# Performance work log

Measured on AMD Instinct MI355X. Metric: run time of the kernel, lower is better.

Reference implementation:

```python
import jax, jax.numpy as jnp
import numpy as np
import math

HIDDEN = 2048
NUM_HEADS = 32
NUM_KV_HEADS = 8
HEAD_DIM = HIDDEN // NUM_HEADS
GROUPS = NUM_HEADS // NUM_KV_HEADS
B, S = 2, 2048


def setup_inputs() -> dict:
    key = jax.random.key(0)
    ks = jax.random.split(key, 9)
    sc = 1.0 / math.sqrt(HIDDEN)
    x = jax.random.normal(ks[0], (B, S, HIDDEN), dtype=jnp.float32)
    # causal mask: 1 where attention allowed, 0 where masked
    mask = jnp.tril(jnp.ones((S, S), dtype=jnp.int32))[None, None, :, :]
    Wq = jax.random.normal(ks[1], (HIDDEN, HIDDEN), dtype=jnp.float32) * sc
    bq = jnp.zeros((HIDDEN,), dtype=jnp.float32)
    Wk = jax.random.normal(ks[2], (NUM_KV_HEADS * HEAD_DIM, HIDDEN), dtype=jnp.float32) * sc
    bk = jnp.zeros((NUM_KV_HEADS * HEAD_DIM,), dtype=jnp.float32)
    Wv = jax.random.normal(ks[3], (NUM_KV_HEADS * HEAD_DIM, HIDDEN), dtype=jnp.float32) * sc
    bv = jnp.zeros((NUM_KV_HEADS * HEAD_DIM,), dtype=jnp.float32)
    Wo = jax.random.normal(ks[4], (HIDDEN, HIDDEN), dtype=jnp.float32) * sc
    bo = jnp.zeros((HIDDEN,), dtype=jnp.float32)
    return {"x": x, "mask": mask, "Wq": Wq, "bq": bq, "Wk": Wk, "bk": bk,
            "Wv": Wv, "bv": bv, "Wo": Wo, "bo": bo}


def reference(x, mask, Wq, bq, Wk, bk, Wv, bv, Wo, bo):
    b, s, _ = x.shape
    # projections (torch Linear: y = x @ W.T + b)
    Q = (x @ Wq.T + bq).reshape(b, s, NUM_HEADS, HEAD_DIM).transpose(0, 2, 1, 3)  # b h s d
    K = (x @ Wk.T + bk).reshape(b, s, NUM_KV_HEADS, HEAD_DIM).transpose(0, 2, 1, 3)
    V = (x @ Wv.T + bv).reshape(b, s, NUM_KV_HEADS, HEAD_DIM).transpose(0, 2, 1, 3)
    # repeat_kv expansion
    K = jnp.repeat(K, GROUPS, axis=1)  # b h s d
    V = jnp.repeat(V, GROUPS, axis=1)
    scores = jnp.einsum('bhqd,bhkd->bhqk', Q, K) / math.sqrt(HEAD_DIM)
    scores = jnp.where(mask == 0, jnp.float32(-jnp.inf), scores)
    w = jax.nn.softmax(scores, axis=-1)
    # dropout is identity in eval mode
    out = jnp.einsum('bhqk,bhkd->bhqd', w, V)
    out = out.transpose(0, 2, 1, 3).reshape(b, s, HIDDEN)
    return out @ Wo.T + bo
```

## Files before the change

### kernel.cpp

```cpp
#include <hip/hip_runtime.h>
#include <hip/hip_bf16.h>
#include <stdint.h>

#define HID   2048
#define SLEN  2048
#define NB    2
#define NHEADS 32
#define NKVH   8
#define HDIM   64
#define KVW    512

typedef __bf16 bf16_t;
typedef __bf16 bf16x4 __attribute__((ext_vector_type(4)));
typedef __bf16 bf16x8 __attribute__((ext_vector_type(8)));
typedef float  f32x4  __attribute__((ext_vector_type(4)));

__device__ __forceinline__ f32x4 mfma16(bf16x8 a, bf16x8 b, f32x4 c) {
  return __builtin_amdgcn_mfma_f32_16x16x32_bf16(a, b, c, 0, 0, 0);
}

__device__ __forceinline__ void gl2lds16(const bf16_t* g, bf16_t* l) {
  __builtin_amdgcn_global_load_lds(
      (const __attribute__((address_space(1))) void*)g,
      (__attribute__((address_space(3))) void*)l,
      16, 0, 0);
}

__device__ __forceinline__ float fast_exp2(float x) {
#if __has_builtin(__builtin_amdgcn_exp2f)
  return __builtin_amdgcn_exp2f(x);
#else
  return __expf(x * 0.69314718f);
#endif
}

__device__ __forceinline__ bf16x8 ld8(const bf16_t* p) {
  return *(const bf16x8*)p;
}
__device__ __forceinline__ bf16x8 ld8(const float* p) {
  f32x4 a = *(const f32x4*)p;
  f32x4 b = *(const f32x4*)(p + 4);
  bf16x8 r;
  r[0] = (bf16_t)a[0]; r[1] = (bf16_t)a[1]; r[2] = (bf16_t)a[2]; r[3] = (bf16_t)a[3];
  r[4] = (bf16_t)b[0]; r[5] = (bf16_t)b[1]; r[6] = (bf16_t)b[2]; r[7] = (bf16_t)b[3];
  return r;
}

__device__ __forceinline__ void st_c(bf16_t* p, float v) { *p = (bf16_t)v; }
__device__ __forceinline__ void st_c(float*  p, float v) { *p = v; }

__global__ __launch_bounds__(256) void cvt_kernel(
    const float* __restrict__ x,  const float* __restrict__ wq,
    const float* __restrict__ wk, const float* __restrict__ wv,
    const float* __restrict__ wo,
    bf16_t* xb, bf16_t* wqb, bf16_t* wkb, bf16_t* wvb, bf16_t* wob)
{
  const float* s; bf16_t* d; size_t n;
  switch (blockIdx.y) {
    case 0:  s = x;  d = xb;  n = (size_t)NB * SLEN * HID; break;
    case 1:  s = wq; d = wqb; n = (size_t)HID * HID; break;
    case 2:  s = wk; d = wkb; n = (size_t)KVW * HID; break;
    case 3:  s = wv; d = wvb; n = (size_t)KVW * HID; break;
    default: s = wo; d = wob; n = (size_t)HID * HID; break;
  }
  const size_t stride = (size_t)gridDim.x * 256 * 8;
  for (size_t i = ((size_t)blockIdx.x * 256 + threadIdx.x) * 8; i < n; i += stride)
    *(bf16x8*)(d + i) = ld8(s + i);
}


__device__ __forceinline__ bf16x8 ldfrag(const bf16_t* __restrict__ Lh, int r, int g) {
  return *(const bf16x8*)(Lh + r * 64 + ((g ^ (r & 7)) << 3));
}

template <int Q>
__device__ __forceinline__ void mfma_quad(const bf16x8 (&af)[2][2],
                                          const bf16x8 (&bfr)[4][2],
                                          f32x4 (&acc)[8][4]) {
#pragma unroll
  for (int ks = 0; ks < 2; ++ks)
#pragma unroll
    for (int i = 0; i < 2; ++i)
#pragma unroll
      for (int ni = 0; ni < 4; ++ni)
        acc[2 * Q + i][ni] = mfma16(af[i][ks], bfr[ni][ks], acc[2 * Q + i][ni]);
}

__device__ __forceinline__ void phase_barrier() {
  __builtin_amdgcn_s_barrier();
  asm volatile("" ::: "memory");
}

__device__ __forceinline__ void gemm256_core(
    const bf16_t* __restrict__ Ag,
    const bf16_t* __restrict__ Bg,
    bf16_t* __restrict__ lds, f32x4 (&acc)[8][4])
{
  const int tid  = threadIdx.x;
  const int lane = tid & 63;
  const int w    = tid >> 6;
  const int fr   = lane & 15;
  const int quad = lane >> 4;
  const int wr   = w >> 2;
  const int wc   = w & 3;
  const int rbB  = (wc & 1) * 64;

  bf16_t* A0 = lds;
  bf16_t* B0 = lds + 16384;
  bf16_t* A1 = lds + 32768;
  bf16_t* B1 = lds + 49152;
  const bf16_t* Ar0 = A0 + wr * 8192;
  const bf16_t* Br0 = B0 + (wc >> 1) * 8192;
  const bf16_t* Ar1 = A1 + wr * 8192;
  const bf16_t* Br1 = B1 + (wc >> 1) * 8192;

  const f32x4 z4 = {0.f, 0.f, 0.f, 0.f};
#pragma unroll
  for (int i = 0; i < 8; ++i)
#pragma unroll
    for (int j = 0; j < 4; ++j) acc[i][j] = z4;

  auto STAGE = [&](const bf16_t* __restrict__ Gp, bf16_t* __restrict__ Lh) {
#pragma unroll
    for (int j = 0; j < 2; ++j) {
      const int s = j * 512 + tid;
      const int r = s >> 3;
      const int g = (s & 7) ^ (r & 7);
      gl2lds16(Gp + (size_t)r * HID + g * 8, Lh + s * 8);
    }
  };

  STAGE(Bg,                  B0);
  STAGE(Bg + 128 * HID,      B0 + 8192);
  STAGE(Ag,                  A0);
  STAGE(Ag + 128 * HID,      A0 + 8192);
  STAGE(Bg + 64,             B1);
  STAGE(Bg + 128 * HID + 64, B1 + 8192);
  asm volatile("s_waitcnt vmcnt(4)" ::: "memory");
  phase_barrier();

  bf16x8 bfr[4][2], af[2][2];

#pragma unroll 1
  for (int it = 0; it < 16; ++it) {
    const bool more = (it < 15);
    const size_t k1 = (size_t)(2 * it + 1) * 64;
    const size_t k2 = (size_t)(2 * it + 2) * 64;
    const size_t k3 = (size_t)(2 * it + 3) * 64;

#pragma unroll
    for (int ni = 0; ni < 4; ++ni)
#pragma unroll
      for (int ks = 0; ks < 2; ++ks)
        bfr[ni][ks] = ldfrag(Br0, rbB + ni * 16 + fr, ks * 4 + quad);
#pragma unroll
    for (int i = 0; i < 2; ++i)
#pragma unroll
      for (int ks = 0; ks < 2; ++ks)
        af[i][ks] = ldfrag(Ar0, i * 16 + fr, ks * 4 + quad);
    STAGE(Ag + k1, A1);
    phase_barrier();
    asm volatile("s_waitcnt lgkmcnt(0)" ::: "memory");
    __builtin_amdgcn_s_setprio(1);
    mfma_quad<0>(af, bfr, acc);
    __builtin_amdgcn_s_setprio(0);
    phase_barrier();

#pragma unroll
    for (int i = 0; i < 2; ++i)
#pragma unroll
      for (int ks = 0; ks < 2; ++ks)
        af[i][ks] = ldfrag(Ar0, 32 + i * 16 + fr, ks * 4 + quad);
    STAGE(Ag + 128 * HID + k1, A1 + 8192);
    phase_barrier();
    asm volatile("s_waitcnt lgkmcnt(0)" ::: "memory");
    __builtin_amdgcn_s_setprio(1);
    mfma_quad<1>(af, bfr, acc);
    __builtin_amdgcn_s_setprio(0);
    phase_barrier();

#pragma unroll
    for (int i = 0; i < 2; ++i)
#pragma unroll
      for (int ks = 0; ks < 2; ++ks)
        af[i][ks] = ldfrag(Ar0, 64 + i * 16 + fr, ks * 4 + quad);
    if (more) STAGE(Bg + k2, B0);
    phase_barrier();
    asm volatile("s_waitcnt lgkmcnt(0)" ::: "memory");
    __builtin_amdgcn_s_setprio(1);
    mfma_quad<2>(af, bfr, acc);
    __builtin_amdgcn_s_setprio(0);
    phase_barrier();

#pragma unroll
    for (int i = 0; i < 2; ++i)
#pragma unroll
      for (int ks = 0; ks < 2; ++ks)
        af[i][ks] = ldfrag(Ar0, 96 + i * 16 + fr, ks * 4 + quad);
    if (more) STAGE(Bg + 128 * HID + k2, B0 + 8192);
    phase_barrier();
    asm volatile("s_waitcnt lgkmcnt(0)" ::: "memory");
    __builtin_amdgcn_s_setprio(1);
    mfma_quad<3>(af, bfr, acc);
    __builtin_amdgcn_s_setprio(0);
    if (more) { asm volatile("s_waitcnt vmcnt(4)" ::: "memory"); }
    else      { asm volatile("s_waitcnt vmcnt(0)" ::: "memory"); }
    phase_barrier();

#pragma unroll
    for (int ni = 0; ni < 4; ++ni)
#pragma unroll
      for (int ks = 0; ks < 2; ++ks)
        bfr[ni][ks] = ldfrag(Br1, rbB + ni * 16 + fr, ks * 4 + quad);
#pragma unroll
    for (int i = 0; i < 2; ++i)
#pragma unroll
      for (int ks = 0; ks < 2; ++ks)
        af[i][ks] = ldfrag(Ar1, i * 16 + fr, ks * 4 + quad);
    if (more) STAGE(Ag + k2, A0);
    phase_barrier();
    asm volatile("s_waitcnt lgkmcnt(0)" ::: "memory");
    __builtin_amdgcn_s_setprio(1);
    mfma_quad<0>(af, bfr, acc);
    __builtin_amdgcn_s_setprio(0);
    phase_barrier();

#pragma unroll
    for (int i = 0; i < 2; ++i)
#pragma unroll
      for (int ks = 0; ks < 2; ++ks)
        af[i][ks] = ldfrag(Ar1, 32 + i * 16 + fr, ks * 4 + quad);
    if (more) STAGE(Ag + 128 * HID + k2, A0 + 8192);
    phase_barrier();
    asm volatile("s_waitcnt lgkmcnt(0)" ::: "memory");
    __builtin_amdgcn_s_setprio(1);
    mfma_quad<1>(af, bfr, acc);
    __builtin_amdgcn_s_setprio(0);
    phase_barrier();

#pragma unroll
    for (int i = 0; i < 2; ++i)
#pragma unroll
      for (int ks = 0; ks < 2; ++ks)
        af[i][ks] = ldfrag(Ar1, 64 + i * 16 + fr, ks * 4 + quad);
    if (more) STAGE(Bg + k3, B1);
    phase_barrier();
    asm volatile("s_waitcnt lgkmcnt(0)" ::: "memory");
    __builtin_amdgcn_s_setprio(1);
    mfma_quad<2>(af, bfr, acc);
    __builtin_amdgcn_s_setprio(0);
    phase_barrier();

#pragma unroll
    for (int i = 0; i < 2; ++i)
#pragma unroll
      for (int ks = 0; ks < 2; ++ks)
        af[i][ks] = ldfrag(Ar1, 96 + i * 16 + fr, ks * 4 + quad);
    if (more) STAGE(Bg + 128 * HID + k3, B1 + 8192);
    phase_barrier();
    asm volatile("s_waitcnt lgkmcnt(0)" ::: "memory");
    __builtin_amdgcn_s_setprio(1);
    mfma_quad<3>(af, bfr, acc);
    __builtin_amdgcn_s_setprio(0);
    if (more) { asm volatile("s_waitcnt vmcnt(4)" ::: "memory"); }
    phase_barrier();
  }
}

__global__ __launch_bounds__(512, 2) void qkv8_kernel(
    const bf16_t* __restrict__ xb, const bf16_t* __restrict__ Wcat,
    const float* __restrict__ bcat,
    bf16_t* __restrict__ Qb, bf16_t* __restrict__ Kb, bf16_t* __restrict__ VbT)
{
  __shared__ __align__(16) bf16_t lds[65536];
  const int cb = blockIdx.x;
  const int mb = blockIdx.y;
  f32x4 acc[8][4];
  gemm256_core(xb + (size_t)mb * 256 * HID, Wcat + (size_t)cb * 256 * HID, lds, acc);

  const int tid = threadIdx.x, lane = tid & 63, w = tid >> 6;
  const int fr = lane & 15, quad = lane >> 4, wr = w >> 2, wc = w & 3;
#pragma unroll
  for (int ni = 0; ni < 4; ++ni) {
    const int gcol = cb * 256 + wc * 64 + ni * 16 + fr;
    const float bz = bcat[gcol];
#pragma unroll
    for (int mi = 0; mi < 8; ++mi) {
      const int grow = mb * 256 + wr * 128 + mi * 16 + quad * 4;
      if (cb < 8) {
#pragma unroll
        for (int r = 0; r < 4; ++r)
          Qb[(size_t)(grow + r) * HID + gcol] = (bf16_t)(acc[mi][ni][r] + bz);
      } else if (cb < 10) {
        const int kc = gcol - 2048;
#pragma unroll
        for (int r = 0; r < 4; ++r)
          Kb[(size_t)(grow + r) * KVW + kc] = (bf16_t)(acc[mi][ni][r] + bz);
      } else {
        const int vc = gcol - 2560;
        const int b = grow >> 11, s = grow & 2047;
        bf16x4 pk;
#pragma unroll
        for (int r = 0; r < 4; ++r) pk[r] = (bf16_t)(acc[mi][ni][r] + bz);
        *(bf16x4*)&VbT[((size_t)(b * NKVH + (vc >> 6)) * HDIM + (vc & 63)) * SLEN + s] = pk;
      }
    }
  }
}

__global__ __launch_bounds__(512, 2) void oproj8_kernel(
    const bf16_t* __restrict__ A, const bf16_t* __restrict__ Wob,
    const float* __restrict__ bo, float* __restrict__ out)
{
  __shared__ __align__(16) bf16_t lds[65536];
  const int cb = blockIdx.x;
  const int mb = blockIdx.y;
  f32x4 acc[8][4];
  gemm256_core(A + (size_t)mb * 256 * HID, Wob + (size_t)cb * 256 * HID, lds, acc);

  const int tid = threadIdx.x, lane = tid & 63, w = tid >> 6;
  const int fr = lane & 15, quad = lane >> 4, wr = w >> 2, wc = w & 3;
#pragma unroll
  for (int ni = 0; ni < 4; ++ni) {
    const int gcol = cb * 256 + wc * 64 + ni * 16 + fr;
    const float bz = bo[gcol];
#pragma unroll
    for (int mi = 0; mi < 8; ++mi) {
      const int grow = mb * 256 + wr * 128 + mi * 16 + quad * 4;
#pragma unroll
      for (int r = 0; r < 4; ++r)
        out[(size_t)(grow + r) * HID + gcol] = acc[mi][ni][r] + bz;
    }
  }
}

template <typename AT, typename CT>
__device__ __forceinline__ void gemm128_tile(
    const AT* __restrict__ Ap, int lda,
    const float* __restrict__ Wp, int ldw,
    const float* __restrict__ biasp,
    CT* __restrict__ Cp, int ldc,
    int K)
{
  __shared__ __align__(16) bf16_t Al[128 * 32];
  __shared__ __align__(16) bf16_t Bl[128 * 32];

  const int tid  = threadIdx.x;
  const int lane = tid & 63;
  const int w    = tid >> 6;
  const int fr   = lane & 15;
  const int quad = lane >> 4;
  const int wm   = (w >> 1) * 64;
  const int wn   = (w & 1) * 64;

  const f32x4 z4 = {0.f, 0.f, 0.f, 0.f};
  f32x4 acc[4][4];
  for (int i = 0; i < 4; ++i)
    for (int j = 0; j < 4; ++j) acc[i][j] = z4;

  const int c0    = w * 2;
  const int srow0 = lane >> 2;
  const int skc   = (lane & 3) * 8;

  for (int k0 = 0; k0 < K; k0 += 32) {
    bf16x8 av[2], bv[2];
    for (int t = 0; t < 2; ++t) {
      const int r = (c0 + t) * 16 + srow0;
      av[t] = ld8(Ap + (size_t)r * lda + k0 + skc);
      bv[t] = ld8(Wp + (size_t)r * ldw + k0 + skc);
    }
    for (int t = 0; t < 2; ++t) {
      const int c = c0 + t;
      *(bf16x8*)&Al[c * 512 + lane * 8] = av[t];
      *(bf16x8*)&Bl[c * 512 + lane * 8] = bv[t];
    }
    __syncthreads();
    bf16x8 af[4], bfr[4];
    for (int mi = 0; mi < 4; ++mi)
      af[mi] = *(const bf16x8*)&Al[(wm + mi * 16 + fr) * 32 + quad * 8];
    for (int ni = 0; ni < 4; ++ni)
      bfr[ni] = *(const bf16x8*)&Bl[(wn + ni * 16 + fr) * 32 + quad * 8];
    for (int mi = 0; mi < 4; ++mi)
      for (int ni = 0; ni < 4; ++ni)
        acc[mi][ni] = mfma16(af[mi], bfr[ni], acc[mi][ni]);
    __syncthreads();
  }

  for (int ni = 0; ni < 4; ++ni) {
    const int col = wn + ni * 16 + fr;
    const float bz = biasp[col];
    for (int mi = 0; mi < 4; ++mi) {
      const int r0 = wm + mi * 16 + quad * 4;
      for (int r = 0; r < 4; ++r)
        st_c(Cp + (size_t)(r0 + r) * ldc + col, acc[mi][ni][r] + bz);
    }
  }
}

__global__ __launch_bounds__(256) void qkv_kernel(
    const float* __restrict__ x,
    const float* __restrict__ Wq, const float* __restrict__ bq,
    const float* __restrict__ Wk, const float* __restrict__ bk,
    const float* __restrict__ Wv, const float* __restrict__ bv,
    bf16_t* Qb, bf16_t* Kb, bf16_t* Vb)
{
  const int nb = blockIdx.x;
  const int mb = blockIdx.y;
  const float* W; const float* bias; bf16_t* C; int ldc;
  if (nb < 16)      { W = Wq + (size_t)nb * 128 * HID;  bias = bq + nb * 128;
                      C = Qb + nb * 128; ldc = HID; }
  else if (nb < 20) { const int j = nb - 16;
                      W = Wk + (size_t)j * 128 * HID;   bias = bk + j * 128;
                      C = Kb + j * 128; ldc = KVW; }
  else              { const int j = nb - 20;
                      W = Wv + (size_t)j * 128 * HID;   bias = bv + j * 128;
                      C = Vb + j * 128; ldc = KVW; }
  gemm128_tile<float, bf16_t>(x + (size_t)mb * 128 * HID, HID, W, HID, bias,
                              C + (size_t)mb * 128 * ldc, ldc, HID);
}

__global__ __launch_bounds__(256) void oproj_kernel(
    const bf16_t* __restrict__ A, const float* __restrict__ Wo,
    const float* __restrict__ bo, float* out)
{
  const int nb = blockIdx.x, mb = blockIdx.y;
  gemm128_tile<bf16_t, float>(A + (size_t)mb * 128 * HID, HID,
                              Wo + (size_t)nb * 128 * HID, HID,
                              bo + nb * 128,
                              out + (size_t)mb * 128 * HID + nb * 128, HID, HID);
}

__global__ __launch_bounds__(256) void vtrans_kernel(
    const bf16_t* __restrict__ Vb, bf16_t* __restrict__ VbT)
{
  __shared__ bf16_t T[64][72];
  const int st = blockIdx.x, kvh = blockIdx.y, b = blockIdx.z;
  const int tid = threadIdx.x;
  {
    const int row = tid >> 2;
    const int c16 = (tid & 3) * 16;
    const bf16_t* src =
        Vb + ((size_t)b * SLEN + st * 64 + row) * KVW + kvh * HDIM + c16;
    *(bf16x8*)&T[row][c16]     = *(const bf16x8*)(src);
    *(bf16x8*)&T[row][c16 + 8] = *(const bf16x8*)(src + 8);
  }
  __syncthreads();
  {
    const int d  = tid >> 2;
    const int sc = (tid & 3) * 16;
    bf16_t tmp[16];
    for (int j = 0; j < 16; ++j) tmp[j] = T[sc + j][d];
    bf16_t* dst = VbT + ((size_t)(b * NKVH + kvh) * HDIM + d) * SLEN + st * 64 + sc;
    *(bf16x8*)dst       = *(bf16x8*)&tmp[0];
    *(bf16x8*)(dst + 8) = *(bf16x8*)&tmp[8];
  }
}

__global__ __launch_bounds__(256) void attn_kernel(
    const bf16_t* Q, const bf16_t* __restrict__ Kg,
    const bf16_t* __restrict__ VT, bf16_t* O)
{
  const int pid = blockIdx.x;
  const int h   = blockIdx.y;
  const int b   = blockIdx.z;
  const int kvh = h >> 2;

  const int tid  = threadIdx.x;
  const int lane = tid & 63;
  const int w    = tid >> 6;
  const int fr   = lane & 15;
  const int quad = lane >> 4;

  const int PS  = 72;
  const int VTS = 136;
  __shared__ __align__(16) bf16_t KL[8192];
  __shared__ __align__(16) bf16_t PP[128 * 72];
  __shared__ __align__(16) bf16_t Vt[64 * 136];

  const size_t qbase = (size_t)b * SLEN;
  const bf16_t* VTh = VT + (size_t)(b * NKVH + kvh) * HDIM * SLEN;

  bf16x8 ones8;
  {
    const bf16_t o1 = (bf16_t)(fr == 0 ? 1.0f : 0.0f);
    for (int j = 0; j < 8; ++j) ones8[j] = o1;
  }

  for (int half = 0; half < 2; ++half) {
    const int qt = half ? (15 - pid) : pid;
    const int q0 = qt * 128;

    bf16x8 qf[2][2];
    for (int qi = 0; qi < 2; ++qi)
      for (int ks = 0; ks < 2; ++ks) {
        const size_t qrow = qbase + q0 + w * 32 + qi * 16 + fr;
        qf[qi][ks] = *(const bf16x8*)&Q[qrow * HID + h * HDIM + ks * 32 + quad * 8];
      }

    const f32x4 z4 = {0.f, 0.f, 0.f, 0.f};
    f32x4 o_acc[2][4];
    f32x4 o_l[2];
    for (int qi = 0; qi < 2; ++qi) {
      o_l[qi] = z4;
      for (int di = 0; di < 4; ++di) o_acc[qi][di] = z4;
    }

    for (int kt = 0; kt <= qt; ++kt) {
      const size_t krow0 = qbase + kt * 128;

      for (int t = 0; t < 4; ++t) {
        const int c  = w * 4 + t;
        const int hf = c >> 3;
        const int r  = (c & 7) * 16 + (lane >> 2);
        const int dk = hf * 32 + (lane & 3) * 8;
        gl2lds16(&Kg[(krow0 + r) * KVW + kvh * HDIM + dk], &KL[c * 512 + lane * 8]);
      }
      {
        const int d  = tid >> 2;
        const int kc = (tid & 3) * 32;
        const bf16_t* src = VTh + (size_t)d * SLEN + kt * 128 + kc;
        bf16x8 v0 = *(const bf16x8*)(src);
        bf16x8 v1 = *(const bf16x8*)(src + 8);
        bf16x8 v2 = *(const bf16x8*)(src + 16);
        bf16x8 v3 = *(const bf16x8*)(src + 24);
        bf16_t* dst = &Vt[d * VTS + kc];
        *(bf16x8*)(dst)      = v0;
        *(bf16x8*)(dst + 8)  = v1;
        *(bf16x8*)(dst + 16) = v2;
        *(bf16x8*)(dst + 24) = v3;
      }
      __syncthreads();

      f32x4 s[2][8];
      for (int qi = 0; qi < 2; ++qi)
        for (int ki = 0; ki < 8; ++ki) s[qi][ki] = z4;
      for (int ks = 0; ks < 2; ++ks)
        for (int ki = 0; ki < 8; ++ki) {
          bf16x8 kf = *(const bf16x8*)&KL[ks * 4096 + (ki * 16 + fr) * 32 + quad * 8];
          s[0][ki] = mfma16(qf[0][ks], kf, s[0][ki]);
          s[1][ki] = mfma16(qf[1][ks], kf, s[1][ki]);
        }

      const float C2 = 0.18033688f;
      const bool diag = (kt == qt);
      for (int hk = 0; hk < 2; ++hk) {
        for (int qi = 0; qi < 2; ++qi)
          for (int k2 = 0; k2 < 4; ++k2) {
            const int ki = hk * 4 + k2;
            for (int r = 0; r < 4; ++r) {
              float pe = fast_exp2(s[qi][ki][r] * C2);
              if (diag && (ki * 16 + fr > w * 32 + qi * 16 + quad * 4 + r))
                pe = 0.f;
              PP[(w * 32 + qi * 16 + quad * 4 + r) * PS + k2 * 16 + fr] =
                  (bf16_t)pe;
            }
          }
        for (int k2 = 0; k2 < 2; ++k2) {
          bf16x8 pf0 = *(const bf16x8*)&PP[(w * 32 + fr) * PS + k2 * 32 + quad * 8];
          bf16x8 pf1 = *(const bf16x8*)&PP[(w * 32 + 16 + fr) * PS + k2 * 32 + quad * 8];
          o_l[0] = mfma16(pf0, ones8, o_l[0]);
          o_l[1] = mfma16(pf1, ones8, o_l[1]);
          const int kb = hk * 64 + k2 * 32;
          for (int di = 0; di < 4; ++di) {
            bf16x8 vf = *(const bf16x8*)&Vt[(di * 16 + fr) * VTS + kb + quad * 8];
            o_acc[0][di] = mfma16(pf0, vf, o_acc[0][di]);
            o_acc[1][di] = mfma16(pf1, vf, o_acc[1][di]);
          }
        }
      }
      __syncthreads();
    }

    for (int qi = 0; qi < 2; ++qi)
      for (int r = 0; r < 4; ++r) {
        const float l  = __shfl(o_l[qi][r], lane & 48);
        const float rl = 1.f / l;
        const size_t qg_ = qbase + q0 + w * 32 + qi * 16 + quad * 4 + r;
        for (int di = 0; di < 4; ++di)
          O[qg_ * HID + h * HDIM + di * 16 + fr] = (bf16_t)(o_acc[qi][di][r] * rl);
      }
  }
}

extern "C" void kernel_launch(void* const* d_in, const int* in_sizes, int n_in,
                              void* d_out, int out_size, void* d_ws, size_t ws_size,
                              hipStream_t stream) {
  const float* x  = (const float*)d_in[0];
  const float* Wq = (const float*)d_in[2];
  const float* bq = (const float*)d_in[3];
  const float* Wk = (const float*)d_in[4];
  const float* bk = (const float*)d_in[5];
  const float* Wv = (const float*)d_in[6];
  const float* bv = (const float*)d_in[7];
  const float* Wo = (const float*)d_in[8];
  const float* bo = (const float*)d_in[9];
  float* out = (float*)d_out;

  const size_t M = (size_t)NB * SLEN;
  dim3 blk(256, 1, 1);

  const size_t needA = (M * HID
                        + (size_t)HID * HID
                        + (size_t)KVW * HID
                        + (size_t)KVW * HID
                        + (size_t)HID * HID
                        + M * HID
                        + M * KVW
                        + M * KVW) * 2
                       + (size_t)(HID + 2 * KVW) * sizeof(float);
  if (ws_size >= needA) {
    bf16_t* xb  = (bf16_t*)d_ws;
    bf16_t* Wqb = xb  + M * HID;
    bf16_t* Wkb = Wqb + (size_t)HID * HID;
    bf16_t* Wvb = Wkb + (size_t)KVW * HID;
    bf16_t* Wob = Wvb + (size_t)KVW * HID;
    bf16_t* Qb  = Wob + (size_t)HID * HID;
    bf16_t* Kb  = Qb  + M * HID;
    bf16_t* VbT = Kb  + M * KVW;
    float*  bcat = (float*)(VbT + M * KVW);

    cvt_kernel<<<dim3(1024, 5, 1), blk, 0, stream>>>(
        x, Wq, Wk, Wv, Wo, xb, Wqb, Wkb, Wvb, Wob);
    hipMemcpyAsync(bcat,             bq, HID * sizeof(float),
                   hipMemcpyDeviceToDevice, stream);
    hipMemcpyAsync(bcat + HID,       bk, KVW * sizeof(float),
                   hipMemcpyDeviceToDevice, stream);
    hipMemcpyAsync(bcat + HID + KVW, bv, KVW * sizeof(float),
                   hipMemcpyDeviceToDevice, stream);
    qkv8_kernel<<<dim3(12, 16, 1), dim3(512, 1, 1), 0, stream>>>(
        xb, Wqb, bcat, Qb, Kb, VbT);
    attn_kernel<<<dim3(8, 32, 2), blk, 0, stream>>>(Qb, Kb, VbT, Qb);
    oproj8_kernel<<<dim3(8, 16, 1), dim3(512, 1, 1), 0, stream>>>(
        Qb, Wob, bo, out);
  } else {
    bf16_t* Qb  = (bf16_t*)d_ws;
    bf16_t* Kb  = Qb + M * HID;
    bf16_t* Vb  = Kb + M * KVW;
    bf16_t* VbT = Vb + M * KVW;

    qkv_kernel<<<dim3(24, 32, 1), blk, 0, stream>>>(x, Wq, bq, Wk, bk, Wv, bv, Qb, Kb, Vb);
    vtrans_kernel<<<dim3(32, 8, 2), blk, 0, stream>>>(Vb, VbT);
    attn_kernel<<<dim3(8, 32, 2), blk, 0, stream>>>(Qb, Kb, VbT, Qb);
    oproj_kernel<<<dim3(16, 32, 1), blk, 0, stream>>>(Qb, Wo, bo, out);
  }
}
```

Before: 323.1 us.

## Restructure attention to 64-row Q tiles with register-resident P via lane shuffles

The attention kernel now processes 64-query tiles, twice as many blocks, with each wave owning 16 rows. It computes S transposed (K as the A operand) so the exp'd probabilities can be packed and exchanged between lanes with shuffles. This replaces the round trip through the shared-memory PP buffer. V is now staged into LDS asynchronously with global_load_lds, and launch bounds ask for 4 blocks per CU to raise occupancy. The bias copies are folded into the conversion kernel in place of three memcpy calls, which cuts launch overhead. In exchange, K/V tiles are reloaded more often per query row, which raises K/V traffic.

```diff
diff --git a/kernel.cpp b/kernel.cpp
--- a/kernel.cpp
+++ b/kernel.cpp
@@ -11,6 +11,7 @@
 #define KVW    512
 
 typedef __bf16 bf16_t;
+typedef __bf16 bf16x2 __attribute__((ext_vector_type(2)));
 typedef __bf16 bf16x4 __attribute__((ext_vector_type(4)));
 typedef __bf16 bf16x8 __attribute__((ext_vector_type(8)));
 typedef float  f32x4  __attribute__((ext_vector_type(4)));
@@ -46,6 +47,11 @@
   return r;
 }
 
+__device__ __forceinline__ uint32_t pack2(float a, float b) {
+  bf16x2 t; t[0] = (bf16_t)a; t[1] = (bf16_t)b;
+  return __builtin_bit_cast(uint32_t, t);
+}
+
 __device__ __forceinline__ void st_c(bf16_t* p, float v) { *p = (bf16_t)v; }
 __device__ __forceinline__ void st_c(float*  p, float v) { *p = v; }
 
@@ -53,8 +59,21 @@
     const float* __restrict__ x,  const float* __restrict__ wq,
     const float* __restrict__ wk, const float* __restrict__ wv,
     const float* __restrict__ wo,
-    bf16_t* xb, bf16_t* wqb, bf16_t* wkb, bf16_t* wvb, bf16_t* wob)
-{
+    const float* __restrict__ bq, const float* __restrict__ bk,
+    const float* __restrict__ bv,
+    bf16_t* xb, bf16_t* wqb, bf16_t* wkb, bf16_t* wvb, bf16_t* wob,
+    float* bcat)
+{
+  if (blockIdx.y >= 5) {
+    const float* fs; float* fd; size_t n;
+    if (blockIdx.y == 5)      { fs = bq; fd = bcat;        n = HID; }
+    else if (blockIdx.y == 6) { fs = bk; fd = bcat + HID;  n = KVW; }
+    else                      { fs = bv; fd = bcat + HID + KVW; n = KVW; }
+    const size_t stride4 = (size_t)gridDim.x * 256 * 4;
+    for (size_t i = ((size_t)blockIdx.x * 256 + threadIdx.x) * 4; i < n; i += stride4)
+      *(f32x4*)(fd + i) = *(const f32x4*)(fs + i);
+    return;
+  }
   const float* s; bf16_t* d; size_t n;
   switch (blockIdx.y) {
     case 0:  s = x;  d = xb;  n = (size_t)NB * SLEN * HID; break;
@@ -67,7 +86,6 @@
   for (size_t i = ((size_t)blockIdx.x * 256 + threadIdx.x) * 8; i < n; i += stride)
     *(bf16x8*)(d + i) = ld8(s + i);
 }
-
 
 __device__ __forceinline__ bf16x8 ldfrag(const bf16_t* __restrict__ Lh, int r, int g) {
   return *(const bf16x8*)(Lh + r * 64 + ((g ^ (r & 7)) << 3));
@@ -456,7 +474,7 @@
   }
 }
 
-__global__ __launch_bounds__(256) void attn_kernel(
+__global__ __launch_bounds__(256, 4) void attn_kernel(
     const bf16_t* Q, const bf16_t* __restrict__ Kg,
     const bf16_t* __restrict__ VT, bf16_t* O)
 {
@@ -471,114 +489,120 @@
   const int fr   = lane & 15;
   const int quad = lane >> 4;
 
-  const int PS  = 72;
-  const int VTS = 136;
   __shared__ __align__(16) bf16_t KL[8192];
-  __shared__ __align__(16) bf16_t PP[128 * 72];
-  __shared__ __align__(16) bf16_t Vt[64 * 136];
+  __shared__ __align__(16) bf16_t VtL[8192];
 
   const size_t qbase = (size_t)b * SLEN;
   const bf16_t* VTh = VT + (size_t)(b * NKVH + kvh) * HDIM * SLEN;
+
+  const int sigma8 = ((quad & 1) << 4) | ((quad & 2) << 2);
+  const bool oddq = (quad & 1);
 
   bf16x8 ones8;
   {
     const bf16_t o1 = (bf16_t)(fr == 0 ? 1.0f : 0.0f);
+#pragma unroll
     for (int j = 0; j < 8; ++j) ones8[j] = o1;
   }
 
   for (int half = 0; half < 2; ++half) {
-    const int qt = half ? (15 - pid) : pid;
-    const int q0 = qt * 128;
-
-    bf16x8 qf[2][2];
-    for (int qi = 0; qi < 2; ++qi)
-      for (int ks = 0; ks < 2; ++ks) {
-        const size_t qrow = qbase + q0 + w * 32 + qi * 16 + fr;
-        qf[qi][ks] = *(const bf16x8*)&Q[qrow * HID + h * HDIM + ks * 32 + quad * 8];
+    const int qt = half ? (31 - pid) : pid;
+    const int q0 = qt * 64;
+
+    bf16x8 qf[2];
+#pragma unroll
+    for (int ks = 0; ks < 2; ++ks)
+      qf[ks] = *(const bf16x8*)&Q[(qbase + q0 + w * 16 + fr) * HID
+                                  + h * HDIM + ks * 32 + quad * 8];
+
+    const f32x4 z4 = {0.f, 0.f, 0.f, 0.f};
+    f32x4 o_acc[4];
+    f32x4 o_l = z4;
+#pragma unroll
+    for (int di = 0; di < 4; ++di) o_acc[di] = z4;
+
+    const int ktmax = qt >> 1;
+    const int qloc  = (qt & 1) * 64 + w * 16 + fr;
+
+    for (int kt = 0; kt <= ktmax; ++kt) {
+      const size_t krow0 = qbase + (size_t)kt * 128;
+
+#pragma unroll
+      for (int j = 0; j < 4; ++j) {
+        const int s  = j * 256 + tid;
+        const int ks = s >> 9, kr = (s >> 2) & 127, c8 = s & 3;
+        gl2lds16(&Kg[(krow0 + kr) * KVW + kvh * HDIM + ks * 32 + c8 * 8],
+                 &KL[s * 8]);
       }
-
-    const f32x4 z4 = {0.f, 0.f, 0.f, 0.f};
-    f32x4 o_acc[2][4];
-    f32x4 o_l[2];
-    for (int qi = 0; qi < 2; ++qi) {
-      o_l[qi] = z4;
-      for (int di = 0; di < 4; ++di) o_acc[qi][di] = z4;
-    }
-
-    for (int kt = 0; kt <= qt; ++kt) {
-      const size_t krow0 = qbase + kt * 128;
-
-      for (int t = 0; t < 4; ++t) {
-        const int c  = w * 4 + t;
-        const int hf = c >> 3;
-        const int r  = (c & 7) * 16 + (lane >> 2);
-        const int dk = hf * 32 + (lane & 3) * 8;
-        gl2lds16(&Kg[(krow0 + r) * KVW + kvh * HDIM + dk], &KL[c * 512 + lane * 8]);
-      }
-      {
-        const int d  = tid >> 2;
-        const int kc = (tid & 3) * 32;
-        const bf16_t* src = VTh + (size_t)d * SLEN + kt * 128 + kc;
-        bf16x8 v0 = *(const bf16x8*)(src);
-        bf16x8 v1 = *(const bf16x8*)(src + 8);
-        bf16x8 v2 = *(const bf16x8*)(src + 16);
-        bf16x8 v3 = *(const bf16x8*)(src + 24);
-        bf16_t* dst = &Vt[d * VTS + kc];
-        *(bf16x8*)(dst)      = v0;
-        *(bf16x8*)(dst + 8)  = v1;
-        *(bf16x8*)(dst + 16) = v2;
-        *(bf16x8*)(dst + 24) = v3;
+#pragma unroll
+      for (int j = 0; j < 4; ++j) {
+        const int idx = j * 256 + tid;
+        const int kb = idx >> 8, d = (idx >> 2) & 63, c8 = idx & 3;
+        gl2lds16(&VTh[(size_t)d * SLEN + kt * 128 + kb * 32 + c8 * 8],
+                 &VtL[idx * 8]);
       }
       __syncthreads();
 
-      f32x4 s[2][8];
-      for (int qi = 0; qi < 2; ++qi)
-        for (int ki = 0; ki < 8; ++ki) s[qi][ki] = z4;
-      for (int ks = 0; ks < 2; ++ks)
+      f32x4 s8[8];
+#pragma unroll
+      for (int ki = 0; ki < 8; ++ki) s8[ki] = z4;
+#pragma unroll
+      for (int ks = 0; ks < 2; ++ks)
+#pragma unroll
         for (int ki = 0; ki < 8; ++ki) {
           bf16x8 kf = *(const bf16x8*)&KL[ks * 4096 + (ki * 16 + fr) * 32 + quad * 8];
-          s[0][ki] = mfma16(qf[0][ks], kf, s[0][ki]);
-          s[1][ki] = mfma16(qf[1][ks], kf, s[1][ki]);
+          s8[ki] = mfma16(kf, qf[ks], s8[ki]);
         }
 
       const float C2 = 0.18033688f;
-      const bool diag = (kt == qt);
-      for (int hk = 0; hk < 2; ++hk) {
-        for (int qi = 0; qi < 2; ++qi)
-          for (int k2 = 0; k2 < 4; ++k2) {
-            const int ki = hk * 4 + k2;
-            for (int r = 0; r < 4; ++r) {
-              float pe = fast_exp2(s[qi][ki][r] * C2);
-              if (diag && (ki * 16 + fr > w * 32 + qi * 16 + quad * 4 + r))
-                pe = 0.f;
-              PP[(w * 32 + qi * 16 + quad * 4 + r) * PS + k2 * 16 + fr] =
-                  (bf16_t)pe;
-            }
+      const bool diag = (kt == ktmax);
+
+#pragma unroll
+      for (int m = 0; m < 4; ++m) {
+        float pe[8];
+#pragma unroll
+        for (int ki2 = 0; ki2 < 2; ++ki2) {
+          const int ki = 2 * m + ki2;
+#pragma unroll
+          for (int r = 0; r < 4; ++r) {
+            float p = fast_exp2(s8[ki][r] * C2);
+            if (diag && (ki * 16 + quad * 4 + r > qloc)) p = 0.f;
+            pe[ki2 * 4 + r] = p;
           }
-        for (int k2 = 0; k2 < 2; ++k2) {
-          bf16x8 pf0 = *(const bf16x8*)&PP[(w * 32 + fr) * PS + k2 * 32 + quad * 8];
-          bf16x8 pf1 = *(const bf16x8*)&PP[(w * 32 + 16 + fr) * PS + k2 * 32 + quad * 8];
-          o_l[0] = mfma16(pf0, ones8, o_l[0]);
-          o_l[1] = mfma16(pf1, ones8, o_l[1]);
-          const int kb = hk * 64 + k2 * 32;
-          for (int di = 0; di < 4; ++di) {
-            bf16x8 vf = *(const bf16x8*)&Vt[(di * 16 + fr) * VTS + kb + quad * 8];
-            o_acc[0][di] = mfma16(pf0, vf, o_acc[0][di]);
-            o_acc[1][di] = mfma16(pf1, vf, o_acc[1][di]);
-          }
+        }
+        uint32_t pw0 = pack2(pe[0], pe[1]);
+        uint32_t pw1 = pack2(pe[2], pe[3]);
+        uint32_t pw2 = pack2(pe[4], pe[5]);
+        uint32_t pw3 = pack2(pe[6], pe[7]);
+        uint32_t x0 = oddq ? pw0 : pw2;
+        uint32_t x1 = oddq ? pw1 : pw3;
+        uint32_t r0 = (uint32_t)__shfl_xor((int)x0, 16);
+        uint32_t r1 = (uint32_t)__shfl_xor((int)x1, 16);
+        union { uint32_t u[4]; bf16x8 v; } pb;
+        pb.u[0] = oddq ? r0 : pw0;
+        pb.u[1] = oddq ? r1 : pw1;
+        pb.u[2] = oddq ? pw2 : r0;
+        pb.u[3] = oddq ? pw3 : r1;
+
+        o_l = mfma16(pb.v, ones8, o_l);
+#pragma unroll
+        for (int di = 0; di < 4; ++di) {
+          bf16x8 vf = *(const bf16x8*)&VtL[m * 2048 + (di * 16 + fr) * 32 + sigma8];
+          o_acc[di] = mfma16(pb.v, vf, o_acc[di]);
         }
       }
       __syncthreads();
     }
 
-    for (int qi = 0; qi < 2; ++qi)
-      for (int r = 0; r < 4; ++r) {
-        const float l  = __shfl(o_l[qi][r], lane & 48);
-        const float rl = 1.f / l;
-        const size_t qg_ = qbase + q0 + w * 32 + qi * 16 + quad * 4 + r;
-        for (int di = 0; di < 4; ++di)
-          O[qg_ * HID + h * HDIM + di * 16 + fr] = (bf16_t)(o_acc[qi][di][r] * rl);
-      }
+#pragma unroll
+    for (int r = 0; r < 4; ++r) {
+      const float l  = __shfl(o_l[r], lane & 48);
+      const float rl = 1.f / l;
+      const size_t qg = qbase + q0 + w * 16 + quad * 4 + r;
+#pragma unroll
+      for (int di = 0; di < 4; ++di)
+        O[qg * HID + h * HDIM + di * 16 + fr] = (bf16_t)(o_acc[di][r] * rl);
+    }
   }
 }
 
@@ -619,17 +643,11 @@
     bf16_t* VbT = Kb  + M * KVW;
     float*  bcat = (float*)(VbT + M * KVW);
 
-    cvt_kernel<<<dim3(1024, 5, 1), blk, 0, stream>>>(
-        x, Wq, Wk, Wv, Wo, xb, Wqb, Wkb, Wvb, Wob);
-    hipMemcpyAsync(bcat,             bq, HID * sizeof(float),
-                   hipMemcpyDeviceToDevice, stream);
-    hipMemcpyAsync(bcat + HID,       bk, KVW * sizeof(float),
-                   hipMemcpyDeviceToDevice, stream);
-    hipMemcpyAsync(bcat + HID + KVW, bv, KVW * sizeof(float),
-                   hipMemcpyDeviceToDevice, stream);
+    cvt_kernel<<<dim3(1024, 8, 1), blk, 0, stream>>>(
+        x, Wq, Wk, Wv, Wo, bq, bk, bv, xb, Wqb, Wkb, Wvb, Wob, bcat);
     qkv8_kernel<<<dim3(12, 16, 1), dim3(512, 1, 1), 0, stream>>>(
         xb, Wqb, bcat, Qb, Kb, VbT);
-    attn_kernel<<<dim3(8, 32, 2), blk, 0, stream>>>(Qb, Kb, VbT, Qb);
+    attn_kernel<<<dim3(16, 32, 2), blk, 0, stream>>>(Qb, Kb, VbT, Qb);
     oproj8_kernel<<<dim3(8, 16, 1), dim3(512, 1, 1), 0, stream>>>(
         Qb, Wob, bo, out);
   } else {
@@ -640,7 +658,7 @@
 
     qkv_kernel<<<dim3(24, 32, 1), blk, 0, stream>>>(x, Wq, bq, Wk, bk, Wv, bv, Qb, Kb, Vb);
     vtrans_kernel<<<dim3(32, 8, 2), blk, 0, stream>>>(Vb, VbT);
-    attn_kernel<<<dim3(8, 32, 2), blk, 0, stream>>>(Qb, Kb, VbT, Qb);
+    attn_kernel<<<dim3(16, 32, 2), blk, 0, stream>>>(Qb, Kb, VbT, Qb);
     oproj_kernel<<<dim3(16, 32, 1), blk, 0, stream>>>(Qb, Wo, bo, out);
   }
 }
```

After: 315.7 us. 1.02x faster.
